# Kernel optimization log

Measured on AMD Instinct MI355X. Metric: run time of the kernel, lower is better.

Reference implementation:

```python
import jax, jax.numpy as jnp
import numpy as np

B, N, C, H = 1, 4096, 512, 8
S = 64  # sqrt(N), static


def setup_inputs() -> dict:
    key = jax.random.key(0)
    ks = jax.random.split(key, 4)
    d = C // H
    return {
        "x": jax.random.normal(ks[0], (B, N, C), dtype=jnp.float32),
        "num_heads": H,
        "bias": jnp.zeros((1,), dtype=jnp.float32),  # unused in original forward
        "scale": jnp.asarray(d ** -0.5, dtype=jnp.float32),
        "Wqkv": jax.random.normal(ks[1], (3 * C, C), dtype=jnp.float32) * (C ** -0.5),
        "bqkv": jnp.zeros((3 * C,), dtype=jnp.float32),
        "Wproj": jax.random.normal(ks[2], (C, C), dtype=jnp.float32) * (C ** -0.5),
        "bproj": jnp.zeros((C,), dtype=jnp.float32),
    }


def reference(x, num_heads, bias, scale, Wqkv, bqkv, Wproj, bproj):
    b, n, c = x.shape
    d = c // num_heads
    # fused QKV projection: [b, n, 3c] -> [3, b, h, n, d]
    qkv = (x @ Wqkv.T + bqkv).reshape(b, n, 3, num_heads, d).transpose(2, 0, 3, 1, 4)
    q, k, v = qkv[0] * scale, qkv[1], qkv[2]
    attn = jax.nn.softmax(jnp.einsum("bhnd,bhmd->bhnm", q, k), axis=-1)
    out = jnp.einsum("bhnm,bhmd->bhnd", attn, v)
    out = out.transpose(0, 2, 1, 3).reshape(b, n, c)
    out = out @ Wproj.T + bproj
    return out.reshape(b, S, S, c)
```

## Files before the change

kernel.cpp:

```cpp
#include <hip/hip_runtime.h>
#include <stdint.h>

#define NTOK 4096
#define CDIM 512
#define HEADS 8
#define DHEAD 64
#define PHEAD (NTOK * DHEAD)
#define LDS_K 72

typedef __bf16 bf16x8 __attribute__((ext_vector_type(8)));
typedef float f32x4 __attribute__((ext_vector_type(4)));

__device__ __forceinline__ unsigned short bfbits(float f) {
    return __builtin_bit_cast(unsigned short, (__bf16)f);
}

__device__ __forceinline__ f32x4 mfma32(bf16x8 a, bf16x8 b, f32x4 c) {
    return __builtin_amdgcn_mfma_f32_16x16x32_bf16(a, b, c, 0, 0, 0);
}

__device__ __forceinline__ void cvt_store8(unsigned short* dst, float4 v0, float4 v1) {
    ushort4 o0, o1;
    o0.x = bfbits(v0.x); o0.y = bfbits(v0.y); o0.z = bfbits(v0.z); o0.w = bfbits(v0.w);
    o1.x = bfbits(v1.x); o1.y = bfbits(v1.y); o1.z = bfbits(v1.z); o1.w = bfbits(v1.w);
    *(ushort4*)dst = o0;
    *(ushort4*)(dst + 4) = o1;
}

__global__ __launch_bounds__(256) void gemm_qkv(
    const float* __restrict__ A,
    const float* __restrict__ Bm,
    const float* __restrict__ bias,
    const float* __restrict__ scale_p,
    unsigned short* __restrict__ qkv_out)
{
    __shared__ __align__(16) unsigned short smem[64 * LDS_K + 128 * LDS_K];
    unsigned short* lA = smem;
    unsigned short* lB = smem + 64 * LDS_K;

    const int tid = threadIdx.x;
    const int mBase = blockIdx.y * 64, nBase = blockIdx.x * 128;
    const int lane = tid & 63;
    const int w = __builtin_amdgcn_readfirstlane(tid >> 6);
    const int l16 = lane & 15, quad = lane >> 4;

    const int rA = tid >> 2, cA = (tid & 3) * 16;
    const int rB = tid >> 1, cB = (tid & 1) * 32;
    const float* pA = &A[(size_t)(mBase + rA) * CDIM + cA];
    const float* pB = &Bm[(size_t)(nBase + rB) * CDIM + cB];

    f32x4 acc[4][2] = {};

    float4 ra[4], rb[8];
    auto issue = [&](int kt) {
#pragma unroll
        for (int u = 0; u < 4; ++u) ra[u] = *(const float4*)(pA + kt + u * 4);
#pragma unroll
        for (int u = 0; u < 8; ++u) rb[u] = *(const float4*)(pB + kt + u * 4);
    };
    issue(0);

    for (int kt = 0; kt < CDIM; kt += 64) {
        __syncthreads();
        cvt_store8(&lA[rA * LDS_K + cA], ra[0], ra[1]);
        cvt_store8(&lA[rA * LDS_K + cA + 8], ra[2], ra[3]);
        cvt_store8(&lB[rB * LDS_K + cB], rb[0], rb[1]);
        cvt_store8(&lB[rB * LDS_K + cB + 8], rb[2], rb[3]);
        cvt_store8(&lB[rB * LDS_K + cB + 16], rb[4], rb[5]);
        cvt_store8(&lB[rB * LDS_K + cB + 24], rb[6], rb[7]);
        __syncthreads();
        if (kt + 64 < CDIM) issue(kt + 64);

#pragma unroll
        for (int kk = 0; kk < 64; kk += 32) {
            bf16x8 af[4], bfr[2];
#pragma unroll
            for (int i = 0; i < 4; ++i)
                af[i] = *(const bf16x8*)&lA[(i * 16 + l16) * LDS_K + kk + quad * 8];
#pragma unroll
            for (int j = 0; j < 2; ++j)
                bfr[j] = *(const bf16x8*)&lB[(w * 32 + j * 16 + l16) * LDS_K + kk + quad * 8];
#pragma unroll
            for (int i = 0; i < 4; ++i)
#pragma unroll
                for (int j = 0; j < 2; ++j)
                    acc[i][j] = mfma32(af[i], bfr[j], acc[i][j]);
        }
    }

    const int three = nBase >> 9;
    const float scl = scale_p[0] * 1.44269504f;
    const float mul = (three == 0) ? scl : 1.0f;

    __syncthreads();
#pragma unroll
    for (int i = 0; i < 4; ++i)
#pragma unroll
        for (int j = 0; j < 2; ++j)
#pragma unroll
            for (int r = 0; r < 4; ++r) {
                const int rl = i * 16 + quad * 4 + r;
                const int cl = w * 32 + j * 16 + l16;
                const float v = (acc[i][j][r] + bias[nBase + cl]) * mul;
                smem[rl * 136 + cl] = bfbits(v);
            }
    __syncthreads();

    const size_t base3 = (size_t)three * (PHEAD * HEADS);
    if (three < 2) {
#pragma unroll
        for (int pass = 0; pass < 4; ++pass) {
            const int idx = pass * 256 + tid;
            const int rl16 = idx & 15, qc = (idx >> 4) & 7;
            const int hsel = (idx >> 7) & 1, t16l = (idx >> 8) & 3;
            const uint4 d = *(const uint4*)&smem[(t16l * 16 + rl16) * 136 + hsel * 64 + qc * 8];
            const int hh = ((nBase >> 6) + hsel) & 7;
            const int t16 = (mBase >> 4) + t16l;
            const size_t dst = base3 + (size_t)hh * PHEAD +
                (size_t)(((t16 * 2 + (qc >> 2)) * 64 + (qc & 3) * 16 + rl16) * 8);
            *(uint4*)&qkv_out[dst] = d;
        }
    } else {
#pragma unroll
        for (int pass = 0; pass < 4; ++pass) {
            const int idx = pass * 256 + tid;
            const int l16t = idx & 15, quadt = (idx >> 4) & 3;
            const int dt = (idx >> 6) & 3, k32l = (idx >> 8) & 1, hsel = (idx >> 9) & 1;
            const int col = hsel * 64 + dt * 16 + l16t;
            unsigned short o8[8];
#pragma unroll
            for (int e = 0; e < 4; ++e) {
                o8[e]     = smem[(k32l * 32 + quadt * 4 + e) * 136 + col];
                o8[e + 4] = smem[(k32l * 32 + 16 + quadt * 4 + e) * 136 + col];
            }
            const int hh = ((nBase >> 6) + hsel) & 7;
            const int k32 = (mBase >> 5) + k32l;
            const size_t dst = base3 + (size_t)hh * PHEAD +
                (size_t)(((k32 * 4 + dt) * 64 + quadt * 16 + l16t) * 8);
            *(uint4*)&qkv_out[dst] = *(uint4*)o8;
        }
    }
}

__global__ __launch_bounds__(256, 2) void flash8_k(
    const unsigned short* __restrict__ qf,
    const unsigned short* __restrict__ kf,
    const unsigned short* __restrict__ vf,
    unsigned short* __restrict__ attn_out)
{
    __shared__ float ldsO[4][64][68];
    __shared__ float sml[4][64];

    const int tid = threadIdx.x;
    const int lane = tid & 63;
    const int w = __builtin_amdgcn_readfirstlane(tid >> 6);
    const int l16 = lane & 15, quad = lane >> 4;
    const int h = blockIdx.x, qb = blockIdx.y;

    const unsigned short* qh = qf + (size_t)h * PHEAD;
    const unsigned short* kb = kf + (size_t)h * PHEAD + w * 65536;
    const unsigned short* vb = vf + (size_t)h * PHEAD + w * 65536;

    bf16x8 qfr[4][2];
#pragma unroll
    for (int qt = 0; qt < 4; ++qt)
#pragma unroll
        for (int d2 = 0; d2 < 2; ++d2)
            qfr[qt][d2] = *(const bf16x8*)&qh[((qb * 4 + qt) * 2 + d2) * 512 + lane * 8];

    f32x4 oacc[4][4] = {};
    float lv[4] = {};

    bf16x8 kA[4], kB[4], vA[4], vB[4];
#pragma unroll
    for (int i = 0; i < 4; ++i) {
        kA[i] = *(const bf16x8*)&kb[i * 512 + lane * 8];
        vA[i] = *(const bf16x8*)&vb[i * 512 + lane * 8];
    }

    auto body = [&](int g, bf16x8* kuse, bf16x8* kload, bf16x8* vuse, bf16x8* vload) {
        const int gn = (g + 1) & 31;
#pragma unroll
        for (int i = 0; i < 4; ++i)
            kload[i] = *(const bf16x8*)&kb[gn * 2048 + i * 512 + lane * 8];
#pragma unroll
        for (int i = 0; i < 4; ++i)
            vload[i] = *(const bf16x8*)&vb[gn * 2048 + i * 512 + lane * 8];

        f32x4 s0[4], s1[4];
        __builtin_amdgcn_s_setprio(1);
#pragma unroll
        for (int qt = 0; qt < 4; ++qt) {
            f32x4 a = {};
            a = mfma32(kuse[0], qfr[qt][0], a);
            a = mfma32(kuse[1], qfr[qt][1], a);
            s0[qt] = a;
            f32x4 b = {};
            b = mfma32(kuse[2], qfr[qt][0], b);
            b = mfma32(kuse[3], qfr[qt][1], b);
            s1[qt] = b;
        }
        __builtin_amdgcn_s_setprio(0);

        bf16x8 pf[4];
#pragma unroll
        for (int qt = 0; qt < 4; ++qt) {
            float e0[4], e1[4];
#pragma unroll
            for (int r = 0; r < 4; ++r) {
                e0[r] = __builtin_amdgcn_exp2f(s0[qt][r]);
                e1[r] = __builtin_amdgcn_exp2f(s1[qt][r]);
            }
            lv[qt] += ((e0[0] + e0[1]) + (e0[2] + e0[3])) +
                      ((e1[0] + e1[1]) + (e1[2] + e1[3]));
            bf16x8 pb;
#pragma unroll
            for (int r = 0; r < 4; ++r) {
                pb[r]     = (__bf16)e0[r];
                pb[4 + r] = (__bf16)e1[r];
            }
            pf[qt] = pb;
        }

        __builtin_amdgcn_s_setprio(1);
#pragma unroll
        for (int dt = 0; dt < 4; ++dt)
#pragma unroll
            for (int qt = 0; qt < 4; ++qt)
                oacc[dt][qt] = mfma32(vuse[dt], pf[qt], oacc[dt][qt]);
        __builtin_amdgcn_s_setprio(0);
    };

    for (int it = 0; it < 16; ++it) {
        body(it * 2 + 0, kA, kB, vA, vB);
        body(it * 2 + 1, kB, kA, vB, vA);
    }

#pragma unroll
    for (int qt = 0; qt < 4; ++qt) {
        float L = lv[qt];
        L += __shfl_xor(L, 16, 64);
        L += __shfl_xor(L, 32, 64);
        if (quad == 0) sml[w][qt * 16 + l16] = L;
    }
#pragma unroll
    for (int qt = 0; qt < 4; ++qt) {
        const int q = qt * 16 + l16;
#pragma unroll
        for (int dt = 0; dt < 4; ++dt)
            *(f32x4*)&ldsO[w][q][dt * 16 + quad * 4] = oacc[dt][qt];
    }
    __syncthreads();
#pragma unroll
    for (int pass = 0; pass < 2; ++pass) {
        const int idx = pass * 256 + tid;
        const int q = idx >> 3, dseg = (idx & 7) * 8;
        const float L = sml[0][q] + sml[1][q] + sml[2][q] + sml[3][q];
        const float inv = 1.f / L;
        unsigned short o8[8];
#pragma unroll
        for (int i = 0; i < 8; ++i) {
            const float v = ldsO[0][q][dseg + i] + ldsO[1][q][dseg + i] +
                            ldsO[2][q][dseg + i] + ldsO[3][q][dseg + i];
            o8[i] = bfbits(v * inv);
        }
        *(uint4*)&attn_out[(size_t)(qb * 64 + q) * CDIM + h * DHEAD + dseg] = *(uint4*)o8;
    }
}

__global__ __launch_bounds__(256) void gemm_proj(
    const unsigned short* __restrict__ A,
    const float* __restrict__ Bm,
    const float* __restrict__ bias,
    float* __restrict__ c_out)
{
    __shared__ __align__(16) unsigned short smem[2 * 64 * LDS_K];
    unsigned short* lA = smem;
    unsigned short* lB = smem + 64 * LDS_K;

    const int tid = threadIdx.x;
    const int mBase = blockIdx.y * 64, nBase = blockIdx.x * 64;
    const int lane = tid & 63;
    const int w = __builtin_amdgcn_readfirstlane(tid >> 6);
    const int l16 = lane & 15, quad = lane >> 4;

    const int rT = tid >> 2, cT = (tid & 3) * 16;
    const unsigned short* pA = &A[(size_t)(mBase + rT) * CDIM + cT];
    const float* pB = &Bm[(size_t)(nBase + rT) * CDIM + cT];

    f32x4 acc[4] = {};

    uint4 rA0, rA1; float4 rb[4];
    auto issue = [&](int kt) {
        rA0 = *(const uint4*)(pA + kt);
        rA1 = *(const uint4*)(pA + kt + 8);
#pragma unroll
        for (int u = 0; u < 4; ++u) rb[u] = *(const float4*)(pB + kt + u * 4);
    };
    issue(0);

    for (int kt = 0; kt < CDIM; kt += 64) {
        __syncthreads();
        *(uint4*)&lA[rT * LDS_K + cT]     = rA0;
        *(uint4*)&lA[rT * LDS_K + cT + 8] = rA1;
        cvt_store8(&lB[rT * LDS_K + cT], rb[0], rb[1]);
        cvt_store8(&lB[rT * LDS_K + cT + 8], rb[2], rb[3]);
        __syncthreads();
        if (kt + 64 < CDIM) issue(kt + 64);

#pragma unroll
        for (int kk = 0; kk < 64; kk += 32) {
            bf16x8 af[4], bfr;
#pragma unroll
            for (int i = 0; i < 4; ++i)
                af[i] = *(const bf16x8*)&lA[(i * 16 + l16) * LDS_K + kk + quad * 8];
            bfr = *(const bf16x8*)&lB[(w * 16 + l16) * LDS_K + kk + quad * 8];
#pragma unroll
            for (int i = 0; i < 4; ++i)
                acc[i] = mfma32(af[i], bfr, acc[i]);
        }
    }

#pragma unroll
    for (int i = 0; i < 4; ++i)
#pragma unroll
        for (int r = 0; r < 4; ++r) {
            const int grow = mBase + i * 16 + quad * 4 + r;
            const int gcol = nBase + w * 16 + l16;
            c_out[(size_t)grow * CDIM + gcol] = acc[i][r] + bias[gcol];
        }
}

extern "C" void kernel_launch(void* const* d_in, const int* in_sizes, int n_in,
                              void* d_out, int out_size, void* d_ws, size_t ws_size,
                              hipStream_t stream) {
    const float* x       = (const float*)d_in[0];
    const float* scale_p = (const float*)d_in[3];
    const float* Wqkv    = (const float*)d_in[4];
    const float* bqkv    = (const float*)d_in[5];
    const float* Wproj   = (const float*)d_in[6];
    const float* bproj   = (const float*)d_in[7];
    float* out = (float*)d_out;

    char* ws = (char*)d_ws;
    const size_t OFF_QKV  = 0;
    const size_t OFF_ATTN = 12582912;
    const size_t NEEDED   = OFF_ATTN + 4194304;
    if (ws_size < NEEDED) return;

    unsigned short* qkvb  = (unsigned short*)(ws + OFF_QKV);
    unsigned short* attnb = (unsigned short*)(ws + OFF_ATTN);

    gemm_qkv<<<dim3(12, 64), 256, 0, stream>>>(x, Wqkv, bqkv, scale_p, qkvb);

    const unsigned short* qfr = qkvb;
    const unsigned short* kfr = qkvb + (size_t)PHEAD * HEADS;
    const unsigned short* vfr = qkvb + (size_t)2 * PHEAD * HEADS;
    flash8_k<<<dim3(8, 64), 256, 0, stream>>>(qfr, kfr, vfr, attnb);

    gemm_proj<<<dim3(8, 64), 256, 0, stream>>>(attnb, Wproj, bproj, out);
}
```

Before: 146.4 us.

## Pre-cast inputs and weights to bf16 once, shrink GEMM K-tile to 32

Adds a single cast kernel that converts x, Wqkv and Wproj to bf16 in workspace. The QKV and projection GEMMs then load bf16 directly, with no per-tile fp32-to-bf16 conversion and half the global load bytes per tile. The K tile drops from 64 to 32 with a smaller LDS stride, so each GEMM runs twice as many barrier-separated iterations. The trade-off is an extra launch plus a round trip through workspace against cheaper GEMM main loops.

```diff
diff --git a/kernel.cpp b/kernel.cpp
--- a/kernel.cpp
+++ b/kernel.cpp
@@ -6,7 +6,7 @@
 #define HEADS 8
 #define DHEAD 64
 #define PHEAD (NTOK * DHEAD)
-#define LDS_K 72
+#define LDS_K 40
 
 typedef __bf16 bf16x8 __attribute__((ext_vector_type(8)));
 typedef float f32x4 __attribute__((ext_vector_type(4)));
@@ -20,21 +20,36 @@
 }
 
 __device__ __forceinline__ void cvt_store8(unsigned short* dst, float4 v0, float4 v1) {
-    ushort4 o0, o1;
-    o0.x = bfbits(v0.x); o0.y = bfbits(v0.y); o0.z = bfbits(v0.z); o0.w = bfbits(v0.w);
-    o1.x = bfbits(v1.x); o1.y = bfbits(v1.y); o1.z = bfbits(v1.z); o1.w = bfbits(v1.w);
-    *(ushort4*)dst = o0;
-    *(ushort4*)(dst + 4) = o1;
+    unsigned short o[8];
+    o[0] = bfbits(v0.x); o[1] = bfbits(v0.y); o[2] = bfbits(v0.z); o[3] = bfbits(v0.w);
+    o[4] = bfbits(v1.x); o[5] = bfbits(v1.y); o[6] = bfbits(v1.z); o[7] = bfbits(v1.w);
+    *(uint4*)dst = *(const uint4*)o;
+}
+
+__global__ __launch_bounds__(256) void cast3_k(
+    const float* __restrict__ x, const float* __restrict__ wq, const float* __restrict__ wp,
+    unsigned short* __restrict__ xb, unsigned short* __restrict__ wqb,
+    unsigned short* __restrict__ wpb)
+{
+    const int b = blockIdx.x;
+    const float* src; unsigned short* dst; int off;
+    if (b < 1024)      { src = x;  dst = xb;  off = b; }
+    else if (b < 1408) { src = wq; dst = wqb; off = b - 1024; }
+    else               { src = wp; dst = wpb; off = b - 1408; }
+    const int i = (off * 256 + threadIdx.x) * 8;
+    const float4 v0 = *(const float4*)(src + i);
+    const float4 v1 = *(const float4*)(src + i + 4);
+    cvt_store8(dst + i, v0, v1);
 }
 
 __global__ __launch_bounds__(256) void gemm_qkv(
-    const float* __restrict__ A,
-    const float* __restrict__ Bm,
+    const unsigned short* __restrict__ A,
+    const unsigned short* __restrict__ Bm,
     const float* __restrict__ bias,
     const float* __restrict__ scale_p,
     unsigned short* __restrict__ qkv_out)
 {
-    __shared__ __align__(16) unsigned short smem[64 * LDS_K + 128 * LDS_K];
+    __shared__ __align__(16) unsigned short smem[64 * 136];
     unsigned short* lA = smem;
     unsigned short* lB = smem + 64 * LDS_K;
 
@@ -43,49 +58,42 @@
     const int lane = tid & 63;
     const int w = __builtin_amdgcn_readfirstlane(tid >> 6);
     const int l16 = lane & 15, quad = lane >> 4;
-
-    const int rA = tid >> 2, cA = (tid & 3) * 16;
-    const int rB = tid >> 1, cB = (tid & 1) * 32;
-    const float* pA = &A[(size_t)(mBase + rA) * CDIM + cA];
-    const float* pB = &Bm[(size_t)(nBase + rB) * CDIM + cB];
+    const int srow = tid >> 2, scol = (tid & 3) * 8;
+
+    const unsigned short* pA  = &A[(size_t)(mBase + srow) * CDIM + scol];
+    const unsigned short* pB0 = &Bm[(size_t)(nBase + srow) * CDIM + scol];
+    const unsigned short* pB1 = &Bm[(size_t)(nBase + 64 + srow) * CDIM + scol];
 
     f32x4 acc[4][2] = {};
 
-    float4 ra[4], rb[8];
+    uint4 rA, rB0, rB1;
     auto issue = [&](int kt) {
-#pragma unroll
-        for (int u = 0; u < 4; ++u) ra[u] = *(const float4*)(pA + kt + u * 4);
-#pragma unroll
-        for (int u = 0; u < 8; ++u) rb[u] = *(const float4*)(pB + kt + u * 4);
+        rA  = *(const uint4*)(pA + kt);
+        rB0 = *(const uint4*)(pB0 + kt);
+        rB1 = *(const uint4*)(pB1 + kt);
     };
     issue(0);
 
-    for (int kt = 0; kt < CDIM; kt += 64) {
+    for (int kt = 0; kt < CDIM; kt += 32) {
         __syncthreads();
-        cvt_store8(&lA[rA * LDS_K + cA], ra[0], ra[1]);
-        cvt_store8(&lA[rA * LDS_K + cA + 8], ra[2], ra[3]);
-        cvt_store8(&lB[rB * LDS_K + cB], rb[0], rb[1]);
-        cvt_store8(&lB[rB * LDS_K + cB + 8], rb[2], rb[3]);
-        cvt_store8(&lB[rB * LDS_K + cB + 16], rb[4], rb[5]);
-        cvt_store8(&lB[rB * LDS_K + cB + 24], rb[6], rb[7]);
+        *(uint4*)&lA[srow * LDS_K + scol]        = rA;
+        *(uint4*)&lB[srow * LDS_K + scol]        = rB0;
+        *(uint4*)&lB[(64 + srow) * LDS_K + scol] = rB1;
         __syncthreads();
-        if (kt + 64 < CDIM) issue(kt + 64);
-
-#pragma unroll
-        for (int kk = 0; kk < 64; kk += 32) {
-            bf16x8 af[4], bfr[2];
-#pragma unroll
-            for (int i = 0; i < 4; ++i)
-                af[i] = *(const bf16x8*)&lA[(i * 16 + l16) * LDS_K + kk + quad * 8];
+        if (kt + 32 < CDIM) issue(kt + 32);
+
+        bf16x8 af[4], bfr[2];
+#pragma unroll
+        for (int i = 0; i < 4; ++i)
+            af[i] = *(const bf16x8*)&lA[(i * 16 + l16) * LDS_K + quad * 8];
+#pragma unroll
+        for (int j = 0; j < 2; ++j)
+            bfr[j] = *(const bf16x8*)&lB[(w * 32 + j * 16 + l16) * LDS_K + quad * 8];
+#pragma unroll
+        for (int i = 0; i < 4; ++i)
 #pragma unroll
             for (int j = 0; j < 2; ++j)
-                bfr[j] = *(const bf16x8*)&lB[(w * 32 + j * 16 + l16) * LDS_K + kk + quad * 8];
-#pragma unroll
-            for (int i = 0; i < 4; ++i)
-#pragma unroll
-                for (int j = 0; j < 2; ++j)
-                    acc[i][j] = mfma32(af[i], bfr[j], acc[i][j]);
-        }
+                acc[i][j] = mfma32(af[i], bfr[j], acc[i][j]);
     }
 
     const int three = nBase >> 9;
@@ -270,7 +278,7 @@
 
 __global__ __launch_bounds__(256) void gemm_proj(
     const unsigned short* __restrict__ A,
-    const float* __restrict__ Bm,
+    const unsigned short* __restrict__ Bm,
     const float* __restrict__ bias,
     float* __restrict__ c_out)
 {
@@ -283,42 +291,35 @@
     const int lane = tid & 63;
     const int w = __builtin_amdgcn_readfirstlane(tid >> 6);
     const int l16 = lane & 15, quad = lane >> 4;
-
-    const int rT = tid >> 2, cT = (tid & 3) * 16;
-    const unsigned short* pA = &A[(size_t)(mBase + rT) * CDIM + cT];
-    const float* pB = &Bm[(size_t)(nBase + rT) * CDIM + cT];
+    const int srow = tid >> 2, scol = (tid & 3) * 8;
+
+    const unsigned short* pA = &A[(size_t)(mBase + srow) * CDIM + scol];
+    const unsigned short* pB = &Bm[(size_t)(nBase + srow) * CDIM + scol];
 
     f32x4 acc[4] = {};
 
-    uint4 rA0, rA1; float4 rb[4];
+    uint4 rA, rB;
     auto issue = [&](int kt) {
-        rA0 = *(const uint4*)(pA + kt);
-        rA1 = *(const uint4*)(pA + kt + 8);
-#pragma unroll
-        for (int u = 0; u < 4; ++u) rb[u] = *(const float4*)(pB + kt + u * 4);
+        rA = *(const uint4*)(pA + kt);
+        rB = *(const uint4*)(pB + kt);
     };
     issue(0);
 
-    for (int kt = 0; kt < CDIM; kt += 64) {
+    for (int kt = 0; kt < CDIM; kt += 32) {
         __syncthreads();
-        *(uint4*)&lA[rT * LDS_K + cT]     = rA0;
-        *(uint4*)&lA[rT * LDS_K + cT + 8] = rA1;
-        cvt_store8(&lB[rT * LDS_K + cT], rb[0], rb[1]);
-        cvt_store8(&lB[rT * LDS_K + cT + 8], rb[2], rb[3]);
+        *(uint4*)&lA[srow * LDS_K + scol] = rA;
+        *(uint4*)&lB[srow * LDS_K + scol] = rB;
         __syncthreads();
-        if (kt + 64 < CDIM) issue(kt + 64);
-
-#pragma unroll
-        for (int kk = 0; kk < 64; kk += 32) {
-            bf16x8 af[4], bfr;
-#pragma unroll
-            for (int i = 0; i < 4; ++i)
-                af[i] = *(const bf16x8*)&lA[(i * 16 + l16) * LDS_K + kk + quad * 8];
-            bfr = *(const bf16x8*)&lB[(w * 16 + l16) * LDS_K + kk + quad * 8];
-#pragma unroll
-            for (int i = 0; i < 4; ++i)
-                acc[i] = mfma32(af[i], bfr, acc[i]);
-        }
+        if (kt + 32 < CDIM) issue(kt + 32);
+
+        bf16x8 af[4], bfr;
+#pragma unroll
+        for (int i = 0; i < 4; ++i)
+            af[i] = *(const bf16x8*)&lA[(i * 16 + l16) * LDS_K + quad * 8];
+        bfr = *(const bf16x8*)&lB[(w * 16 + l16) * LDS_K + quad * 8];
+#pragma unroll
+        for (int i = 0; i < 4; ++i)
+            acc[i] = mfma32(af[i], bfr, acc[i]);
     }
 
 #pragma unroll
@@ -345,18 +346,26 @@
     char* ws = (char*)d_ws;
     const size_t OFF_QKV  = 0;
     const size_t OFF_ATTN = 12582912;
-    const size_t NEEDED   = OFF_ATTN + 4194304;
+    const size_t OFF_XB   = 16777216;
+    const size_t OFF_WQB  = 20971520;
+    const size_t OFF_WPB  = 22544384;
+    const size_t NEEDED   = OFF_WPB + 524288;
     if (ws_size < NEEDED) return;
 
     unsigned short* qkvb  = (unsigned short*)(ws + OFF_QKV);
     unsigned short* attnb = (unsigned short*)(ws + OFF_ATTN);
-
-    gemm_qkv<<<dim3(12, 64), 256, 0, stream>>>(x, Wqkv, bqkv, scale_p, qkvb);
+    unsigned short* xb    = (unsigned short*)(ws + OFF_XB);
+    unsigned short* wqb   = (unsigned short*)(ws + OFF_WQB);
+    unsigned short* wpb   = (unsigned short*)(ws + OFF_WPB);
+
+    cast3_k<<<1536, 256, 0, stream>>>(x, Wqkv, Wproj, xb, wqb, wpb);
+
+    gemm_qkv<<<dim3(12, 64), 256, 0, stream>>>(xb, wqb, bqkv, scale_p, qkvb);
 
     const unsigned short* qfr = qkvb;
     const unsigned short* kfr = qkvb + (size_t)PHEAD * HEADS;
     const unsigned short* vfr = qkvb + (size_t)2 * PHEAD * HEADS;
     flash8_k<<<dim3(8, 64), 256, 0, stream>>>(qfr, kfr, vfr, attnb);
 
-    gemm_proj<<<dim3(8, 64), 256, 0, stream>>>(attnb, Wproj, bproj, out);
-}
+    gemm_proj<<<dim3(8, 64), 256, 0, stream>>>(attnb, wpb, bproj, out);
+}
```

After: 132.0 us. -9.9%, faster.
